# Optimization experiments

Measured on AMD Instinct MI355X. Metric: run time of the kernel, lower is better.

Reference implementation:

```python
import jax, jax.numpy as jnp
import numpy as np

B, T, M = 65536, 512, 12  # series, timesteps, seasonal period


def setup_inputs() -> dict:
    key = jax.random.key(0)
    kx, = jax.random.split(key, 1)
    x = jax.random.uniform(kx, (B, T, 1), dtype=jnp.float32) + 0.5  # positive series values
    init_alpha = 0.5 / M
    alpha = jnp.full((1, 1), init_alpha, dtype=jnp.float32)
    beta = jnp.full((1, 1), 0.1 * init_alpha, dtype=jnp.float32)
    phi = jnp.full((1, 1), 0.99, dtype=jnp.float32)
    gamma = jnp.full((1, 1), 0.5, dtype=jnp.float32)
    l0 = jnp.ones((B, 1), dtype=jnp.float32)
    b0 = jnp.zeros((B, 1), dtype=jnp.float32)
    s0 = jnp.ones((B, M), dtype=jnp.float32)
    return {"x": x, "alpha": alpha, "beta": beta, "phi": phi,
            "gamma": gamma, "l0": l0, "b0": b0, "s0": s0}


def reference(x, alpha, beta, phi, gamma, l0, b0, s0):
    # Holt-Winters ESRNN cell: additive trend, multiplicative season, period M.
    # Per step (matching the seasonal+trend branch of the Keras cell):
    #   l = a*(x/s0[:, :1]) + (1-a)*(l0 + b0*phi)
    #   b = be*(l - l0) + (1-be)*(b0*phi)
    #   s_new = g*(x/(l + b*phi)) + (1-g)*s0[:, :1]
    #   s = concat(s0[:,1:], s_new)
    #   out = (l + b*phi) * s0[:, 1:2]
    def step(carry, x_t):
        l_p, b_p, s_p = carry              # (B,1), (B,1), (B,M)
        lb_p = l_p + b_p * phi             # damped trend forecast of level
        l = alpha * (x_t / s_p[:, :1]) + (1.0 - alpha) * lb_p
        b = beta * (l - l_p) + (1.0 - beta) * (b_p * phi)
        s_new = gamma * (x_t / (l + b * phi)) + (1.0 - gamma) * s_p[:, :1]
        s = jnp.concatenate([s_p[:, 1:], s_new], axis=1)
        out = (l + b * phi) * s_p[:, 1:2]
        return (l, b, s), out

    x_tm = jnp.transpose(x, (1, 0, 2))     # (T,B,1) time-major for scan
    _, outs = jax.lax.scan(step, (l0, b0, s0), x_tm)
    return jnp.transpose(outs, (1, 0, 2))  # (B,T,1)
```

## Files before the change

### kernel.cpp

```cpp
#include <hip/hip_runtime.h>


constexpr int TT     = 512;
constexpr int TC     = 48;
constexpr int NCH    = 10;
constexpr int SW     = 64;
constexpr int LST    = 65;
constexpr int PITCH4 = TT / 4;

#define LDS_FENCE() asm volatile("s_waitcnt lgkmcnt(0)" ::: "memory")

#define STEPM(XV, SH, SN, OV)                                              \
    do {                                                                   \
        const float s_h_ = ring[SH];                                       \
        const float q_   = (XV) * __builtin_amdgcn_rcpf(s_h_);             \
        const float lb_  = fmaf(b, phi, l);                                \
        const float ln_  = fmaf(alpha, q_, omal * lb_);                    \
        const float bphi_ = b * phi;                                       \
        const float bn_  = fmaf(beta, ln_ - l, ombe * bphi_);              \
        const float lb2_ = fmaf(bn_, phi, ln_);                            \
        const float sn_  = fmaf(gamma, (XV) * __builtin_amdgcn_rcpf(lb2_), \
                                omg * s_h_);                               \
        (OV) = lb2_ * ring[SN];                                            \
        ring[SH] = sn_;                                                    \
        l = ln_; b = bn_;                                                  \
    } while (0)

__global__ __launch_bounds__(64) void esrnn_kernel(
    const float* __restrict__ x,
    const float* __restrict__ p_alpha,
    const float* __restrict__ p_beta,
    const float* __restrict__ p_phi,
    const float* __restrict__ p_gamma,
    const float* __restrict__ l0,
    const float* __restrict__ b0,
    const float* __restrict__ s0,
    float* __restrict__ out)
{
    const int tid = threadIdx.x;
    const int series0 = blockIdx.x * SW;
    const int i = series0 + tid;

    __shared__ float lds_x[TC * LST];
    __shared__ float lds_o[TC * LST];

    const float alpha = p_alpha[0];
    const float beta  = p_beta[0];
    const float phi   = p_phi[0];
    const float gamma = p_gamma[0];
    const float omal  = 1.0f - alpha;
    const float ombe  = 1.0f - beta;
    const float omg   = 1.0f - gamma;

    float l = l0[i];
    float b = b0[i];

    float ring[12];
    {
        const float4* s04 = reinterpret_cast<const float4*>(s0 + (size_t)i * 12);
        float4 sa = s04[0], sb = s04[1], sc = s04[2];
        ring[0] = sa.x; ring[1] = sa.y; ring[2]  = sa.z; ring[3]  = sa.w;
        ring[4] = sb.x; ring[5] = sb.y; ring[6]  = sb.z; ring[7]  = sb.w;
        ring[8] = sc.x; ring[9] = sc.y; ring[10] = sc.z; ring[11] = sc.w;
    }

    int rr[12], qq[12];
    #pragma unroll
    for (int m = 0; m < 12; ++m) {
        const int f = tid + SW * m;
        rr[m] = f / 12;
        qq[m] = f - 12 * rr[m];
    }
    int rt[8], qt[8];
    #pragma unroll
    for (int m = 0; m < 8; ++m) {
        const int f = tid + SW * m;
        rt[m] = f >> 3;
        qt[m] = f & 7;
    }

    const float4* x4 = reinterpret_cast<const float4*>(x) + (size_t)series0 * PITCH4;
    float4*       o4 = reinterpret_cast<float4*>(out)     + (size_t)series0 * PITCH4;

    float4 vx[12], vn[12];

    #pragma unroll
    for (int m = 0; m < 12; ++m)
        vx[m] = x4[(size_t)rr[m] * PITCH4 + qq[m]];

    #pragma unroll 1
    for (int k = 0; k < NCH; ++k) {
        #pragma unroll
        for (int m = 0; m < 12; ++m) {
            const int cb = qq[m] * 4;
            lds_x[(cb + 0) * LST + rr[m]] = vx[m].x;
            lds_x[(cb + 1) * LST + rr[m]] = vx[m].y;
            lds_x[(cb + 2) * LST + rr[m]] = vx[m].z;
            lds_x[(cb + 3) * LST + rr[m]] = vx[m].w;
        }

        if (k < NCH - 1) {
            #pragma unroll
            for (int m = 0; m < 12; ++m)
                vn[m] = x4[(size_t)rr[m] * PITCH4 + (k + 1) * 12 + qq[m]];
        } else {
            #pragma unroll
            for (int m = 0; m < 8; ++m)
                vn[m] = x4[(size_t)rt[m] * PITCH4 + 120 + qt[m]];
        }

        LDS_FENCE();

        #pragma unroll
        for (int s = 0; s < TC; ++s) {
            const int sh  = s % 12;
            const int sn2 = (s + 1) % 12;
            const float xv = lds_x[s * LST + tid];
            float ov;
            STEPM(xv, sh, sn2, ov);
            lds_o[s * LST + tid] = ov;
        }

        LDS_FENCE();

        #pragma unroll
        for (int m = 0; m < 12; ++m) {
            const int cb = qq[m] * 4;
            float4 o;
            o.x = lds_o[(cb + 0) * LST + rr[m]];
            o.y = lds_o[(cb + 1) * LST + rr[m]];
            o.z = lds_o[(cb + 2) * LST + rr[m]];
            o.w = lds_o[(cb + 3) * LST + rr[m]];
            o4[(size_t)rr[m] * PITCH4 + k * 12 + qq[m]] = o;
        }

        #pragma unroll
        for (int m = 0; m < 12; ++m) vx[m] = vn[m];
    }

    {
        #pragma unroll
        for (int m = 0; m < 8; ++m) {
            const int cb = qt[m] * 4;
            lds_x[(cb + 0) * LST + rt[m]] = vx[m].x;
            lds_x[(cb + 1) * LST + rt[m]] = vx[m].y;
            lds_x[(cb + 2) * LST + rt[m]] = vx[m].z;
            lds_x[(cb + 3) * LST + rt[m]] = vx[m].w;
        }
        LDS_FENCE();
        #pragma unroll
        for (int s = 0; s < 32; ++s) {
            const int sh  = s % 12;
            const int sn2 = (s + 1) % 12;
            const float xv = lds_x[s * LST + tid];
            float ov;
            STEPM(xv, sh, sn2, ov);
            lds_o[s * LST + tid] = ov;
        }
        LDS_FENCE();
        #pragma unroll
        for (int m = 0; m < 8; ++m) {
            const int cb = qt[m] * 4;
            float4 o;
            o.x = lds_o[(cb + 0) * LST + rt[m]];
            o.y = lds_o[(cb + 1) * LST + rt[m]];
            o.z = lds_o[(cb + 2) * LST + rt[m]];
            o.w = lds_o[(cb + 3) * LST + rt[m]];
            o4[(size_t)rt[m] * PITCH4 + 120 + qt[m]] = o;
        }
    }
}

extern "C" void kernel_launch(void* const* d_in, const int* in_sizes, int n_in,
                              void* d_out, int out_size, void* d_ws, size_t ws_size,
                              hipStream_t stream)
{
    const float* x       = (const float*)d_in[0];
    const float* p_alpha = (const float*)d_in[1];
    const float* p_beta  = (const float*)d_in[2];
    const float* p_phi   = (const float*)d_in[3];
    const float* p_gamma = (const float*)d_in[4];
    const float* l0      = (const float*)d_in[5];
    const float* b0      = (const float*)d_in[6];
    const float* s0      = (const float*)d_in[7];
    float* out = (float*)d_out;

    const int B = in_sizes[5];
    const int grid = B / SW;

    esrnn_kernel<<<grid, SW, 0, stream>>>(x, p_alpha, p_beta, p_phi, p_gamma,
                                          l0, b0, s0, out);
}
```

Before: 56.48 us.

## Deepen global prefetch to two chunks and use nontemporal output stores

Adds a third register buffer so x loads for chunk k+2 are issued while chunk k is computed, giving the memory system more time to hide latency. The explicit lgkmcnt waits become compiler-only barriers, leaving the compiler to insert the LDS waits it needs within the single wave. Output stores become nontemporal to avoid polluting the cache. The extra 12 float4 registers per thread raise register pressure, which could lower occupancy.

```diff
diff --git a/kernel.cpp b/kernel.cpp
--- a/kernel.cpp
+++ b/kernel.cpp
@@ -8,7 +8,9 @@
 constexpr int LST    = 65;
 constexpr int PITCH4 = TT / 4;
 
-#define LDS_FENCE() asm volatile("s_waitcnt lgkmcnt(0)" ::: "memory")
+typedef float f32x4 __attribute__((ext_vector_type(4)));
+
+#define CBAR() asm volatile("" ::: "memory")
 
 #define STEPM(XV, SH, SN, OV)                                              \
     do {                                                                   \
@@ -80,13 +82,16 @@
     }
 
     const float4* x4 = reinterpret_cast<const float4*>(x) + (size_t)series0 * PITCH4;
-    float4*       o4 = reinterpret_cast<float4*>(out)     + (size_t)series0 * PITCH4;
+    f32x4*        o4 = reinterpret_cast<f32x4*>(out)      + (size_t)series0 * PITCH4;
 
-    float4 vx[12], vn[12];
+    float4 vx[12], vn[12], vm[12];
 
     #pragma unroll
     for (int m = 0; m < 12; ++m)
         vx[m] = x4[(size_t)rr[m] * PITCH4 + qq[m]];
+    #pragma unroll
+    for (int m = 0; m < 12; ++m)
+        vn[m] = x4[(size_t)rr[m] * PITCH4 + 12 + qq[m]];
 
     #pragma unroll 1
     for (int k = 0; k < NCH; ++k) {
@@ -98,18 +103,18 @@
             lds_x[(cb + 2) * LST + rr[m]] = vx[m].z;
             lds_x[(cb + 3) * LST + rr[m]] = vx[m].w;
         }
+        CBAR();
 
-        if (k < NCH - 1) {
+        if (k < NCH - 2) {
             #pragma unroll
             for (int m = 0; m < 12; ++m)
-                vn[m] = x4[(size_t)rr[m] * PITCH4 + (k + 1) * 12 + qq[m]];
-        } else {
+                vm[m] = x4[(size_t)rr[m] * PITCH4 + (k + 2) * 12 + qq[m]];
+        } else if (k == NCH - 2) {
             #pragma unroll
             for (int m = 0; m < 8; ++m)
-                vn[m] = x4[(size_t)rt[m] * PITCH4 + 120 + qt[m]];
+                vm[m] = x4[(size_t)rt[m] * PITCH4 + 120 + qt[m]];
         }
-
-        LDS_FENCE();
+        CBAR();
 
         #pragma unroll
         for (int s = 0; s < TC; ++s) {
@@ -120,22 +125,22 @@
             STEPM(xv, sh, sn2, ov);
             lds_o[s * LST + tid] = ov;
         }
-
-        LDS_FENCE();
+        CBAR();
 
         #pragma unroll
         for (int m = 0; m < 12; ++m) {
             const int cb = qq[m] * 4;
-            float4 o;
+            f32x4 o;
             o.x = lds_o[(cb + 0) * LST + rr[m]];
             o.y = lds_o[(cb + 1) * LST + rr[m]];
             o.z = lds_o[(cb + 2) * LST + rr[m]];
             o.w = lds_o[(cb + 3) * LST + rr[m]];
-            o4[(size_t)rr[m] * PITCH4 + k * 12 + qq[m]] = o;
+            __builtin_nontemporal_store(o, &o4[(size_t)rr[m] * PITCH4 + k * 12 + qq[m]]);
         }
+        CBAR();
 
         #pragma unroll
-        for (int m = 0; m < 12; ++m) vx[m] = vn[m];
+        for (int m = 0; m < 12; ++m) { vx[m] = vn[m]; vn[m] = vm[m]; }
     }
 
     {
@@ -147,7 +152,7 @@
             lds_x[(cb + 2) * LST + rt[m]] = vx[m].z;
             lds_x[(cb + 3) * LST + rt[m]] = vx[m].w;
         }
-        LDS_FENCE();
+        CBAR();
         #pragma unroll
         for (int s = 0; s < 32; ++s) {
             const int sh  = s % 12;
@@ -157,16 +162,16 @@
             STEPM(xv, sh, sn2, ov);
             lds_o[s * LST + tid] = ov;
         }
-        LDS_FENCE();
+        CBAR();
         #pragma unroll
         for (int m = 0; m < 8; ++m) {
             const int cb = qt[m] * 4;
-            float4 o;
+            f32x4 o;
             o.x = lds_o[(cb + 0) * LST + rt[m]];
             o.y = lds_o[(cb + 1) * LST + rt[m]];
             o.z = lds_o[(cb + 2) * LST + rt[m]];
             o.w = lds_o[(cb + 3) * LST + rt[m]];
-            o4[(size_t)rt[m] * PITCH4 + 120 + qt[m]] = o;
+            __builtin_nontemporal_store(o, &o4[(size_t)rt[m] * PITCH4 + 120 + qt[m]]);
         }
     }
 }
```

Result: faster. 47.64 us (-15.6%).
